# Optimization experiments

Hardware: AMD Instinct MI355X
Metric: run time of the kernel (lower is better)

The kernel has to match this reference:

```python
import jax, jax.numpy as jnp
import numpy as np

EPS = 1e-3


def interpolate_dim(x, n_out):
    # linear interpolation along axis 1, align_corners=True (matches F.interpolate linear)
    n_in = x.shape[1]
    pos = jnp.linspace(0.0, n_in - 1.0, n_out)
    idx0 = jnp.floor(pos).astype(jnp.int32)
    idx1 = jnp.minimum(idx0 + 1, n_in - 1)
    w = (pos - idx0.astype(x.dtype))[None, :, None]
    return x[:, idx0] * (1.0 - w) + x[:, idx1] * w


def logits_to_a_coeff(a_logits, eps):
    # stability-triangle parameterization: |a1| < 2, |a1| - 1 < a2 < 1
    stab = 1.0 - eps
    a1 = 2.0 * jnp.tanh(a_logits[..., 0]) * stab
    a1_abs = jnp.abs(a1)
    a2 = 0.5 * ((2.0 - a1_abs) * jnp.tanh(a_logits[..., 1]) * stab + a1_abs)
    return jnp.stack([a1, a2], axis=-1)  # (B, T, 2)


def sample_wise_lpc(x, a_coeff):
    # time-varying all-pole: y[t] = x[t] - a1[t]*y[t-1] - a2[t]*y[t-2]
    bs = x.shape[0]
    xs = (x.T, a_coeff[..., 0].T, a_coeff[..., 1].T)  # (T, B) each

    def step(carry, inp):
        y1, y2 = carry
        xt, a1, a2 = inp
        y = xt - a1 * y1 - a2 * y2
        return (y, y1), y

    zero = jnp.zeros((bs,), x.dtype)
    _, ys = jax.lax.scan(step, (zero, zero), xs)
    return ys.T  # (B, T)


def time_varying_fir(y, b_coeff):
    # y_out[t] = b0[t]*y[t] + b1[t]*y[t-1] + b2[t]*y[t-2], zero initial conditions
    y_pad = jnp.pad(y, ((0, 0), (2, 0)))
    return (b_coeff[..., 0] * y
            + b_coeff[..., 1] * y_pad[:, 1:-1]
            + b_coeff[..., 2] * y_pad[:, :-2])


def setup_inputs() -> dict:
    key = jax.random.key(0)
    k1, k2 = jax.random.split(key)
    x = jax.random.normal(k1, (32, 262144), dtype=jnp.float32)
    coeff_logits = jax.random.normal(k2, (32, 256, 5), dtype=jnp.float32)
    return {"x": x, "coeff_logits": coeff_logits}


def reference(x, coeff_logits):
    n_samples = x.shape[1]
    # interp_coeff=False: interpolate logits to sample rate first
    logits = interpolate_dim(coeff_logits, n_samples)  # (B, n_samples, 5)
    a_coeff = logits_to_a_coeff(logits[..., :2], EPS)  # (B, n_samples, 2)
    b_coeff = logits[..., 2:]                          # (B, n_samples, 3)
    y_a = sample_wise_lpc(x, a_coeff)
    y_ab = time_varying_fir(y_a, b_coeff)
    return y_ab
```

## Files before the change

kernel.cpp:

```cpp
#include <hip/hip_runtime.h>
#include <math.h>

#define BATCH 32
#define NSAMP 262144
#define NKNOT 256
#define EPSV  0.001f
#define CH    16
#define CPB   256
#define SPB   (CH * CPB)
#define NCROW (NSAMP / CH)
#define BPR   (NCROW / CPB)
#define NB    (BATCH * BPR)
#define NWAVE (CPB / 64)
#define TSTRIDE (CPB + 2)

__device__ __forceinline__ float fast_tanh(float x) {
    float e = __expf(2.0f * x);
    float r = __builtin_amdgcn_rcpf(e + 1.0f);
    return fmaf(-2.0f, r, 1.0f);
}

__global__ __launch_bounds__(256, 4) void k_agg(
    const float* __restrict__ x,
    const float* __restrict__ cl,
    float* __restrict__ G)
{
    __shared__ float tile[CH][TSTRIDE];
    __shared__ float wag[NWAVE][6];
    const int tid = threadIdx.x;
    const int b = blockIdx.x;
    const int lane = tid & 63, wid = tid >> 6;

    const float4* x4 = (const float4*)x + (size_t)b * (SPB / 4);
    #pragma unroll
    for (int i = 0; i < SPB / 4 / CPB; ++i) {
        int ii = tid + i * CPB;
        float4 v = x4[ii];
        int idx = ii << 2;
        int cc = idx >> 4, qq = idx & 15;
        tile[qq + 0][cc] = v.x;
        tile[qq + 1][cc] = v.y;
        tile[qq + 2][cc] = v.z;
        tile[qq + 3][cc] = v.w;
    }

    int chunk = b * CPB + tid;
    int r = chunk >> 14;
    int c = chunk & (NCROW - 1);
    const float scale = 255.0f / 262143.0f;
    float pos0 = (float)(c * CH) * scale;
    float fiA = floorf(pos0);
    int idxA = (int)fiA;
    float w0v = pos0 - fiA;
    const float* kb = cl + (size_t)r * NKNOT * 5;
    int i1 = min(idxA + 1, NKNOT - 1);
    int i2 = min(idxA + 2, NKNOT - 1);
    float k00 = kb[idxA*5+0], k01 = kb[i1*5+0], k02 = kb[i2*5+0];
    float k10 = kb[idxA*5+1], k11 = kb[i1*5+1], k12 = kb[i2*5+1];

    __syncthreads();

    const float stab = 1.0f - EPSV, stab2 = 2.0f * stab;
    float p1 = 0.f, p2 = 0.f, A1 = 1.f, A2 = 0.f, B1 = 0.f, B2 = 1.f;
    #pragma unroll
    for (int j = 0; j < CH; ++j) {
        float xs = tile[j][tid];
        float w = fmaf((float)j, scale, w0v);
        bool sel = w >= 1.0f;
        float wu = sel ? w - 1.0f : w;
        float l0a = sel ? k01 : k00, l0b = sel ? k02 : k01;
        float l1a = sel ? k11 : k10, l1b = sel ? k12 : k11;
        float l0 = fmaf(wu, l0b - l0a, l0a);
        float l1 = fmaf(wu, l1b - l1a, l1a);
        float a1 = stab2 * fast_tanh(l0);
        float a1a = fabsf(a1);
        float a2 = 0.5f * fmaf((2.0f - a1a) * stab, fast_tanh(l1), a1a);
        float p  = fmaf(-a2, p2, xs);  p = fmaf(-a1, p1, p);
        float hA = fmaf(-a1, A1, -a2 * A2);
        float hB = fmaf(-a1, B1, -a2 * B2);
        p2 = p1; p1 = p;
        A2 = A1; A1 = hA;
        B2 = B1; B1 = hB;
    }
    float L00 = A1, L01 = B1, L10 = A2, L11 = B2, Lv0 = p1, Lv1 = p2;

    #pragma unroll
    for (int d = 1; d < 64; d <<= 1) {
        float o00 = __shfl_up(L00, d), o01 = __shfl_up(L01, d);
        float o10 = __shfl_up(L10, d), o11 = __shfl_up(L11, d);
        float ov0 = __shfl_up(Lv0, d), ov1 = __shfl_up(Lv1, d);
        if (lane >= d) {
            float n00 = L00 * o00 + L01 * o10;
            float n01 = L00 * o01 + L01 * o11;
            float n10 = L10 * o00 + L11 * o10;
            float n11 = L10 * o01 + L11 * o11;
            float nv0 = fmaf(L00, ov0, fmaf(L01, ov1, Lv0));
            float nv1 = fmaf(L10, ov0, fmaf(L11, ov1, Lv1));
            L00 = n00; L01 = n01; L10 = n10; L11 = n11; Lv0 = nv0; Lv1 = nv1;
        }
    }
    if (lane == 63) {
        wag[wid][0] = L00; wag[wid][1] = L01; wag[wid][2] = L10;
        wag[wid][3] = L11; wag[wid][4] = Lv0; wag[wid][5] = Lv1;
    }
    __syncthreads();

    if (tid == CPB - 1) {
        float P00 = 1.f, P01 = 0.f, P10 = 0.f, P11 = 1.f, Pv0 = 0.f, Pv1 = 0.f;
        for (int w2 = 0; w2 < NWAVE - 1; ++w2) {
            float a00 = wag[w2][0], a01 = wag[w2][1], a10 = wag[w2][2];
            float a11 = wag[w2][3], av0 = wag[w2][4], av1 = wag[w2][5];
            float n00 = a00 * P00 + a01 * P10;
            float n01 = a00 * P01 + a01 * P11;
            float n10 = a10 * P00 + a11 * P10;
            float n11 = a10 * P01 + a11 * P11;
            float nv0 = fmaf(a00, Pv0, fmaf(a01, Pv1, av0));
            float nv1 = fmaf(a10, Pv0, fmaf(a11, Pv1, av1));
            P00 = n00; P01 = n01; P10 = n10; P11 = n11; Pv0 = nv0; Pv1 = nv1;
        }
        G[b*6+0] = L00 * P00 + L01 * P10;
        G[b*6+1] = L00 * P01 + L01 * P11;
        G[b*6+2] = L10 * P00 + L11 * P10;
        G[b*6+3] = L10 * P01 + L11 * P11;
        G[b*6+4] = fmaf(L00, Pv0, fmaf(L01, Pv1, Lv0));
        G[b*6+5] = fmaf(L10, Pv0, fmaf(L11, Pv1, Lv1));
    }
}

__global__ __launch_bounds__(64) void k_rowscan(
    const float* __restrict__ G,
    float* __restrict__ S)
{
    int r = blockIdx.x;
    int lane = threadIdx.x;
    int rowFirst = r * BPR;
    int k = rowFirst + lane;
    float A00 = G[k*6+0], A01 = G[k*6+1], A10 = G[k*6+2];
    float A11 = G[k*6+3], Av0 = G[k*6+4], Av1 = G[k*6+5];
    #pragma unroll
    for (int d = 1; d < BPR; d <<= 1) {
        float o00 = __shfl_up(A00, d), o01 = __shfl_up(A01, d);
        float o10 = __shfl_up(A10, d), o11 = __shfl_up(A11, d);
        float ov0 = __shfl_up(Av0, d), ov1 = __shfl_up(Av1, d);
        if (lane >= d) {
            float n00 = A00 * o00 + A01 * o10;
            float n01 = A00 * o01 + A01 * o11;
            float n10 = A10 * o00 + A11 * o10;
            float n11 = A10 * o01 + A11 * o11;
            float nv0 = fmaf(A00, ov0, fmaf(A01, ov1, Av0));
            float nv1 = fmaf(A10, ov0, fmaf(A11, ov1, Av1));
            A00 = n00; A01 = n01; A10 = n10; A11 = n11; Av0 = nv0; Av1 = nv1;
        }
    }
    float e0 = __shfl_up(Av0, 1);
    float e1 = __shfl_up(Av1, 1);
    if (lane == 0) { e0 = 0.f; e1 = 0.f; }
    S[k*2 + 0] = e0;
    S[k*2 + 1] = e1;
}

__global__ __launch_bounds__(256, 4) void k_apply(
    const float* __restrict__ x,
    const float* __restrict__ cl,
    const float* __restrict__ S,
    float* __restrict__ out)
{
    __shared__ float tile[CH][TSTRIDE];
    __shared__ float wag[NWAVE][6];
    const int tid = threadIdx.x;
    const int b = blockIdx.x;
    const int lane = tid & 63, wid = tid >> 6;

    const float4* x4 = (const float4*)x + (size_t)b * (SPB / 4);
    #pragma unroll
    for (int i = 0; i < SPB / 4 / CPB; ++i) {
        int ii = tid + i * CPB;
        float4 v = x4[ii];
        int idx = ii << 2;
        int cc = idx >> 4, qq = idx & 15;
        tile[qq + 0][cc] = v.x;
        tile[qq + 1][cc] = v.y;
        tile[qq + 2][cc] = v.z;
        tile[qq + 3][cc] = v.w;
    }

    int chunk = b * CPB + tid;
    int r = chunk >> 14;
    int c = chunk & (NCROW - 1);
    const float scale = 255.0f / 262143.0f;
    float pos0 = (float)(c * CH) * scale;
    float fiA = floorf(pos0);
    int idxA = (int)fiA;
    float w0v = pos0 - fiA;
    const float* kb = cl + (size_t)r * NKNOT * 5;
    int i1 = min(idxA + 1, NKNOT - 1);
    int i2 = min(idxA + 2, NKNOT - 1);
    float k00 = kb[idxA*5+0], k01 = kb[i1*5+0], k02 = kb[i2*5+0];
    float k10 = kb[idxA*5+1], k11 = kb[i1*5+1], k12 = kb[i2*5+1];
    float k20 = kb[idxA*5+2], k21 = kb[i1*5+2], k22 = kb[i2*5+2];
    float k30 = kb[idxA*5+3], k31 = kb[i1*5+3], k32 = kb[i2*5+3];
    float k40 = kb[idxA*5+4], k41 = kb[i1*5+4], k42 = kb[i2*5+4];

    __syncthreads();

    const float stab = 1.0f - EPSV, stab2 = 2.0f * stab;
    float p1 = 0.f, p2 = 0.f, A1 = 1.f, A2 = 0.f, B1 = 0.f, B2 = 1.f;
    #pragma unroll
    for (int j = 0; j < CH; ++j) {
        float xs = tile[j][tid];
        float w = fmaf((float)j, scale, w0v);
        bool sel = w >= 1.0f;
        float wu = sel ? w - 1.0f : w;
        float l0a = sel ? k01 : k00, l0b = sel ? k02 : k01;
        float l1a = sel ? k11 : k10, l1b = sel ? k12 : k11;
        float l0 = fmaf(wu, l0b - l0a, l0a);
        float l1 = fmaf(wu, l1b - l1a, l1a);
        float a1 = stab2 * fast_tanh(l0);
        float a1a = fabsf(a1);
        float a2 = 0.5f * fmaf((2.0f - a1a) * stab, fast_tanh(l1), a1a);
        float p  = fmaf(-a2, p2, xs);  p = fmaf(-a1, p1, p);
        float hA = fmaf(-a1, A1, -a2 * A2);
        float hB = fmaf(-a1, B1, -a2 * B2);
        p2 = p1; p1 = p;
        A2 = A1; A1 = hA;
        B2 = B1; B1 = hB;
    }
    float L00 = A1, L01 = B1, L10 = A2, L11 = B2, Lv0 = p1, Lv1 = p2;

    #pragma unroll
    for (int d = 1; d < 64; d <<= 1) {
        float o00 = __shfl_up(L00, d), o01 = __shfl_up(L01, d);
        float o10 = __shfl_up(L10, d), o11 = __shfl_up(L11, d);
        float ov0 = __shfl_up(Lv0, d), ov1 = __shfl_up(Lv1, d);
        if (lane >= d) {
            float n00 = L00 * o00 + L01 * o10;
            float n01 = L00 * o01 + L01 * o11;
            float n10 = L10 * o00 + L11 * o10;
            float n11 = L10 * o01 + L11 * o11;
            float nv0 = fmaf(L00, ov0, fmaf(L01, ov1, Lv0));
            float nv1 = fmaf(L10, ov0, fmaf(L11, ov1, Lv1));
            L00 = n00; L01 = n01; L10 = n10; L11 = n11; Lv0 = nv0; Lv1 = nv1;
        }
    }
    if (lane == 63) {
        wag[wid][0] = L00; wag[wid][1] = L01; wag[wid][2] = L10;
        wag[wid][3] = L11; wag[wid][4] = Lv0; wag[wid][5] = Lv1;
    }
    __syncthreads();
    float P00 = 1.f, P01 = 0.f, P10 = 0.f, P11 = 1.f, Pv0 = 0.f, Pv1 = 0.f;
    for (int w2 = 0; w2 < wid; ++w2) {
        float a00 = wag[w2][0], a01 = wag[w2][1], a10 = wag[w2][2];
        float a11 = wag[w2][3], av0 = wag[w2][4], av1 = wag[w2][5];
        float n00 = a00 * P00 + a01 * P10;
        float n01 = a00 * P01 + a01 * P11;
        float n10 = a10 * P00 + a11 * P10;
        float n11 = a10 * P01 + a11 * P11;
        float nv0 = fmaf(a00, Pv0, fmaf(a01, Pv1, av0));
        float nv1 = fmaf(a10, Pv0, fmaf(a11, Pv1, av1));
        P00 = n00; P01 = n01; P10 = n10; P11 = n11; Pv0 = nv0; Pv1 = nv1;
    }
    float E00 = __shfl_up(L00, 1), E01 = __shfl_up(L01, 1);
    float E10 = __shfl_up(L10, 1), E11 = __shfl_up(L11, 1);
    float Ev0 = __shfl_up(Lv0, 1), Ev1 = __shfl_up(Lv1, 1);
    if (lane == 0) { E00 = 1.f; E01 = 0.f; E10 = 0.f; E11 = 1.f; Ev0 = 0.f; Ev1 = 0.f; }
    float C00 = E00 * P00 + E01 * P10;
    float C01 = E00 * P01 + E01 * P11;
    float C10 = E10 * P00 + E11 * P10;
    float C11 = E10 * P01 + E11 * P11;
    float Cv0 = fmaf(E00, Pv0, fmaf(E01, Pv1, Ev0));
    float Cv1 = fmaf(E10, Pv0, fmaf(E11, Pv1, Ev1));

    float s0 = S[b*2+0], s1 = S[b*2+1];
    float y1 = fmaf(C00, s0, fmaf(C01, s1, Cv0));
    float y2 = fmaf(C10, s0, fmaf(C11, s1, Cv1));

    #pragma unroll
    for (int j = 0; j < CH; ++j) {
        float xs = tile[j][tid];
        float w = fmaf((float)j, scale, w0v);
        bool sel = w >= 1.0f;
        float wu = sel ? w - 1.0f : w;
        float l0a = sel ? k01 : k00, l0b = sel ? k02 : k01;
        float l1a = sel ? k11 : k10, l1b = sel ? k12 : k11;
        float b0a = sel ? k21 : k20, b0b = sel ? k22 : k21;
        float b1a = sel ? k31 : k30, b1b = sel ? k32 : k31;
        float b2a = sel ? k41 : k40, b2b = sel ? k42 : k41;
        float l0 = fmaf(wu, l0b - l0a, l0a);
        float l1 = fmaf(wu, l1b - l1a, l1a);
        float b0 = fmaf(wu, b0b - b0a, b0a);
        float b1 = fmaf(wu, b1b - b1a, b1a);
        float b2 = fmaf(wu, b2b - b2a, b2a);
        float a1 = stab2 * fast_tanh(l0);
        float a1a = fabsf(a1);
        float a2 = 0.5f * fmaf((2.0f - a1a) * stab, fast_tanh(l1), a1a);
        float y = fmaf(-a2, y2, xs);  y = fmaf(-a1, y1, y);
        tile[j][tid] = fmaf(b0, y, fmaf(b1, y1, b2 * y2));
        y2 = y1; y1 = y;
    }
    __syncthreads();

    float4* out4 = (float4*)out + (size_t)b * (SPB / 4);
    #pragma unroll
    for (int i = 0; i < SPB / 4 / CPB; ++i) {
        int ii = tid + i * CPB;
        int idx = ii << 2;
        int cc = idx >> 4, qq = idx & 15;
        float4 v;
        v.x = tile[qq + 0][cc];
        v.y = tile[qq + 1][cc];
        v.z = tile[qq + 2][cc];
        v.w = tile[qq + 3][cc];
        out4[ii] = v;
    }
}

extern "C" void kernel_launch(void* const* d_in, const int* in_sizes, int n_in,
                              void* d_out, int out_size, void* d_ws, size_t ws_size,
                              hipStream_t stream) {
    const float* x  = (const float*)d_in[0];
    const float* cl = (const float*)d_in[1];
    float* out = (float*)d_out;
    float* G = (float*)d_ws;
    float* S = G + (size_t)NB * 6;

    hipLaunchKernelGGL(k_agg,     dim3(NB),    dim3(CPB), 0, stream, x, cl, G);
    hipLaunchKernelGGL(k_rowscan, dim3(BATCH), dim3(64),  0, stream, G, S);
    hipLaunchKernelGGL(k_apply,   dim3(NB),    dim3(CPB), 0, stream, x, cl, S, out);
}
```

Baseline: 42.68 us.

## Fuse row scan into apply, use exp recurrence for tanh, row-major float4 LDS tile

The separate row-scan kernel is removed, and every apply block's first wave redoes the 64-block prefix scan over the aggregates, which are now stored in SoA layout. This saves one launch and its serialization at the cost of redundant work. Per-sample tanh now multiplies the exponential by a constant ratio inside each knot segment instead of calling expf per sample, replacing the exp with a multiply. The LDS tile moves to a padded row-per-thread layout so threads use float4 reads and writes. The recurrent exp product may add small float drift.

```diff
diff --git a/kernel.cpp b/kernel.cpp
--- a/kernel.cpp
+++ b/kernel.cpp
@@ -12,20 +12,14 @@
 #define BPR   (NCROW / CPB)
 #define NB    (BATCH * BPR)
 #define NWAVE (CPB / 64)
-#define TSTRIDE (CPB + 2)
-
-__device__ __forceinline__ float fast_tanh(float x) {
-    float e = __expf(2.0f * x);
-    float r = __builtin_amdgcn_rcpf(e + 1.0f);
-    return fmaf(-2.0f, r, 1.0f);
-}
+#define ROWW  20
 
 __global__ __launch_bounds__(256, 4) void k_agg(
     const float* __restrict__ x,
     const float* __restrict__ cl,
     float* __restrict__ G)
 {
-    __shared__ float tile[CH][TSTRIDE];
+    __shared__ float tile[CPB * ROWW];
     __shared__ float wag[NWAVE][6];
     const int tid = threadIdx.x;
     const int b = blockIdx.x;
@@ -33,15 +27,10 @@
 
     const float4* x4 = (const float4*)x + (size_t)b * (SPB / 4);
     #pragma unroll
-    for (int i = 0; i < SPB / 4 / CPB; ++i) {
+    for (int i = 0; i < 4; ++i) {
         int ii = tid + i * CPB;
         float4 v = x4[ii];
-        int idx = ii << 2;
-        int cc = idx >> 4, qq = idx & 15;
-        tile[qq + 0][cc] = v.x;
-        tile[qq + 1][cc] = v.y;
-        tile[qq + 2][cc] = v.z;
-        tile[qq + 3][cc] = v.w;
+        *(float4*)&tile[(ii >> 2) * ROWW + ((ii & 3) << 2)] = v;
     }
 
     int chunk = b * CPB + tid;
@@ -58,29 +47,54 @@
     float k00 = kb[idxA*5+0], k01 = kb[i1*5+0], k02 = kb[i2*5+0];
     float k10 = kb[idxA*5+1], k11 = kb[i1*5+1], k12 = kb[i2*5+1];
 
+    int jb = 0;
+    #pragma unroll
+    for (int j = 0; j < CH; ++j) jb += (fmaf((float)j, scale, w0v) < 1.0f) ? 1 : 0;
+
+    float dA0 = k01 - k00, dB0 = k02 - k01;
+    float dA1 = k11 - k10, dB1 = k12 - k11;
+    float wb  = fmaf((float)jb, scale, w0v) - 1.0f;
+    float eA0 = __expf(2.0f * fmaf(w0v, dA0, k00));
+    float EA0 = __expf(2.0f * scale * dA0);
+    float eB0 = __expf(2.0f * fmaf(wb,  dB0, k01));
+    float EB0 = __expf(2.0f * scale * dB0);
+    float eA1 = __expf(2.0f * fmaf(w0v, dA1, k10));
+    float EA1 = __expf(2.0f * scale * dA1);
+    float eB1 = __expf(2.0f * fmaf(wb,  dB1, k11));
+    float EB1 = __expf(2.0f * scale * dB1);
+
     __syncthreads();
 
     const float stab = 1.0f - EPSV, stab2 = 2.0f * stab;
     float p1 = 0.f, p2 = 0.f, A1 = 1.f, A2 = 0.f, B1 = 0.f, B2 = 1.f;
-    #pragma unroll
-    for (int j = 0; j < CH; ++j) {
-        float xs = tile[j][tid];
-        float w = fmaf((float)j, scale, w0v);
-        bool sel = w >= 1.0f;
-        float wu = sel ? w - 1.0f : w;
-        float l0a = sel ? k01 : k00, l0b = sel ? k02 : k01;
-        float l1a = sel ? k11 : k10, l1b = sel ? k12 : k11;
-        float l0 = fmaf(wu, l0b - l0a, l0a);
-        float l1 = fmaf(wu, l1b - l1a, l1a);
-        float a1 = stab2 * fast_tanh(l0);
-        float a1a = fabsf(a1);
-        float a2 = 0.5f * fmaf((2.0f - a1a) * stab, fast_tanh(l1), a1a);
-        float p  = fmaf(-a2, p2, xs);  p = fmaf(-a1, p1, p);
-        float hA = fmaf(-a1, A1, -a2 * A2);
-        float hB = fmaf(-a1, B1, -a2 * B2);
-        p2 = p1; p1 = p;
-        A2 = A1; A1 = hA;
-        B2 = B1; B1 = hB;
+    float e0 = eA0, e1 = eA1;
+    #pragma unroll
+    for (int jj = 0; jj < CH / 4; ++jj) {
+        float4 xq = *(const float4*)&tile[tid * ROWW + (jj << 2)];
+        #pragma unroll
+        for (int q = 0; q < 4; ++q) {
+            const int j = jj * 4 + q;
+            if (j > 0) {
+                float m0 = (j <= jb) ? EA0 : EB0;
+                float m1 = (j <= jb) ? EA1 : EB1;
+                e0 = (j == jb) ? eB0 : e0 * m0;
+                e1 = (j == jb) ? eB1 : e1 * m1;
+            }
+            float r0 = __builtin_amdgcn_rcpf(e0 + 1.0f);
+            float r1 = __builtin_amdgcn_rcpf(e1 + 1.0f);
+            float th0 = fmaf(-2.0f, r0, 1.0f);
+            float th1 = fmaf(-2.0f, r1, 1.0f);
+            float a1 = stab2 * th0;
+            float a1a = fabsf(a1);
+            float a2 = 0.5f * fmaf((2.0f - a1a) * stab, th1, a1a);
+            float xs = (&xq.x)[q];
+            float p  = fmaf(-a2, p2, xs);  p = fmaf(-a1, p1, p);
+            float hA = fmaf(-a1, A1, -a2 * A2);
+            float hB = fmaf(-a1, B1, -a2 * B2);
+            p2 = p1; p1 = p;
+            A2 = A1; A1 = hA;
+            B2 = B1; B1 = hB;
+        }
     }
     float L00 = A1, L01 = B1, L10 = A2, L11 = B2, Lv0 = p1, Lv1 = p2;
 
@@ -118,70 +132,64 @@
             float nv1 = fmaf(a10, Pv0, fmaf(a11, Pv1, av1));
             P00 = n00; P01 = n01; P10 = n10; P11 = n11; Pv0 = nv0; Pv1 = nv1;
         }
-        G[b*6+0] = L00 * P00 + L01 * P10;
-        G[b*6+1] = L00 * P01 + L01 * P11;
-        G[b*6+2] = L10 * P00 + L11 * P10;
-        G[b*6+3] = L10 * P01 + L11 * P11;
-        G[b*6+4] = fmaf(L00, Pv0, fmaf(L01, Pv1, Lv0));
-        G[b*6+5] = fmaf(L10, Pv0, fmaf(L11, Pv1, Lv1));
-    }
-}
-
-__global__ __launch_bounds__(64) void k_rowscan(
-    const float* __restrict__ G,
-    float* __restrict__ S)
-{
-    int r = blockIdx.x;
-    int lane = threadIdx.x;
-    int rowFirst = r * BPR;
-    int k = rowFirst + lane;
-    float A00 = G[k*6+0], A01 = G[k*6+1], A10 = G[k*6+2];
-    float A11 = G[k*6+3], Av0 = G[k*6+4], Av1 = G[k*6+5];
-    #pragma unroll
-    for (int d = 1; d < BPR; d <<= 1) {
-        float o00 = __shfl_up(A00, d), o01 = __shfl_up(A01, d);
-        float o10 = __shfl_up(A10, d), o11 = __shfl_up(A11, d);
-        float ov0 = __shfl_up(Av0, d), ov1 = __shfl_up(Av1, d);
-        if (lane >= d) {
-            float n00 = A00 * o00 + A01 * o10;
-            float n01 = A00 * o01 + A01 * o11;
-            float n10 = A10 * o00 + A11 * o10;
-            float n11 = A10 * o01 + A11 * o11;
-            float nv0 = fmaf(A00, ov0, fmaf(A01, ov1, Av0));
-            float nv1 = fmaf(A10, ov0, fmaf(A11, ov1, Av1));
-            A00 = n00; A01 = n01; A10 = n10; A11 = n11; Av0 = nv0; Av1 = nv1;
-        }
-    }
-    float e0 = __shfl_up(Av0, 1);
-    float e1 = __shfl_up(Av1, 1);
-    if (lane == 0) { e0 = 0.f; e1 = 0.f; }
-    S[k*2 + 0] = e0;
-    S[k*2 + 1] = e1;
+        G[0*NB + b] = L00 * P00 + L01 * P10;
+        G[1*NB + b] = L00 * P01 + L01 * P11;
+        G[2*NB + b] = L10 * P00 + L11 * P10;
+        G[3*NB + b] = L10 * P01 + L11 * P11;
+        G[4*NB + b] = fmaf(L00, Pv0, fmaf(L01, Pv1, Lv0));
+        G[5*NB + b] = fmaf(L10, Pv0, fmaf(L11, Pv1, Lv1));
+    }
 }
 
 __global__ __launch_bounds__(256, 4) void k_apply(
     const float* __restrict__ x,
     const float* __restrict__ cl,
-    const float* __restrict__ S,
+    const float* __restrict__ G,
     float* __restrict__ out)
 {
-    __shared__ float tile[CH][TSTRIDE];
+    __shared__ float tile[CPB * ROWW];
     __shared__ float wag[NWAVE][6];
+    __shared__ float sInit[2];
     const int tid = threadIdx.x;
     const int b = blockIdx.x;
     const int lane = tid & 63, wid = tid >> 6;
 
     const float4* x4 = (const float4*)x + (size_t)b * (SPB / 4);
     #pragma unroll
-    for (int i = 0; i < SPB / 4 / CPB; ++i) {
+    for (int i = 0; i < 4; ++i) {
         int ii = tid + i * CPB;
         float4 v = x4[ii];
-        int idx = ii << 2;
-        int cc = idx >> 4, qq = idx & 15;
-        tile[qq + 0][cc] = v.x;
-        tile[qq + 1][cc] = v.y;
-        tile[qq + 2][cc] = v.z;
-        tile[qq + 3][cc] = v.w;
+        *(float4*)&tile[(ii >> 2) * ROWW + ((ii & 3) << 2)] = v;
+    }
+
+    if (wid == 0) {
+        int rowFirst = b & ~(BPR - 1);
+        int k = rowFirst + lane;
+        float A00 = G[0*NB + k], A01 = G[1*NB + k], A10 = G[2*NB + k];
+        float A11 = G[3*NB + k], Av0 = G[4*NB + k], Av1 = G[5*NB + k];
+        #pragma unroll
+        for (int d = 1; d < 64; d <<= 1) {
+            float o00 = __shfl_up(A00, d), o01 = __shfl_up(A01, d);
+            float o10 = __shfl_up(A10, d), o11 = __shfl_up(A11, d);
+            float ov0 = __shfl_up(Av0, d), ov1 = __shfl_up(Av1, d);
+            if (lane >= d) {
+                float n00 = A00 * o00 + A01 * o10;
+                float n01 = A00 * o01 + A01 * o11;
+                float n10 = A10 * o00 + A11 * o10;
+                float n11 = A10 * o01 + A11 * o11;
+                float nv0 = fmaf(A00, ov0, fmaf(A01, ov1, Av0));
+                float nv1 = fmaf(A10, ov0, fmaf(A11, ov1, Av1));
+                A00 = n00; A01 = n01; A10 = n10; A11 = n11; Av0 = nv0; Av1 = nv1;
+            }
+        }
+        int myIdx = b & (BPR - 1);
+        int src = (myIdx > 0) ? myIdx - 1 : 0;
+        float s0 = __shfl(Av0, src);
+        float s1 = __shfl(Av1, src);
+        if (lane == 0) {
+            sInit[0] = myIdx ? s0 : 0.f;
+            sInit[1] = myIdx ? s1 : 0.f;
+        }
     }
 
     int chunk = b * CPB + tid;
@@ -201,29 +209,54 @@
     float k30 = kb[idxA*5+3], k31 = kb[i1*5+3], k32 = kb[i2*5+3];
     float k40 = kb[idxA*5+4], k41 = kb[i1*5+4], k42 = kb[i2*5+4];
 
+    int jb = 0;
+    #pragma unroll
+    for (int j = 0; j < CH; ++j) jb += (fmaf((float)j, scale, w0v) < 1.0f) ? 1 : 0;
+
+    float dA0 = k01 - k00, dB0 = k02 - k01;
+    float dA1 = k11 - k10, dB1 = k12 - k11;
+    float wb  = fmaf((float)jb, scale, w0v) - 1.0f;
+    float eA0 = __expf(2.0f * fmaf(w0v, dA0, k00));
+    float EA0 = __expf(2.0f * scale * dA0);
+    float eB0 = __expf(2.0f * fmaf(wb,  dB0, k01));
+    float EB0 = __expf(2.0f * scale * dB0);
+    float eA1 = __expf(2.0f * fmaf(w0v, dA1, k10));
+    float EA1 = __expf(2.0f * scale * dA1);
+    float eB1 = __expf(2.0f * fmaf(wb,  dB1, k11));
+    float EB1 = __expf(2.0f * scale * dB1);
+
     __syncthreads();
 
     const float stab = 1.0f - EPSV, stab2 = 2.0f * stab;
     float p1 = 0.f, p2 = 0.f, A1 = 1.f, A2 = 0.f, B1 = 0.f, B2 = 1.f;
-    #pragma unroll
-    for (int j = 0; j < CH; ++j) {
-        float xs = tile[j][tid];
-        float w = fmaf((float)j, scale, w0v);
-        bool sel = w >= 1.0f;
-        float wu = sel ? w - 1.0f : w;
-        float l0a = sel ? k01 : k00, l0b = sel ? k02 : k01;
-        float l1a = sel ? k11 : k10, l1b = sel ? k12 : k11;
-        float l0 = fmaf(wu, l0b - l0a, l0a);
-        float l1 = fmaf(wu, l1b - l1a, l1a);
-        float a1 = stab2 * fast_tanh(l0);
-        float a1a = fabsf(a1);
-        float a2 = 0.5f * fmaf((2.0f - a1a) * stab, fast_tanh(l1), a1a);
-        float p  = fmaf(-a2, p2, xs);  p = fmaf(-a1, p1, p);
-        float hA = fmaf(-a1, A1, -a2 * A2);
-        float hB = fmaf(-a1, B1, -a2 * B2);
-        p2 = p1; p1 = p;
-        A2 = A1; A1 = hA;
-        B2 = B1; B1 = hB;
+    float e0 = eA0, e1 = eA1;
+    #pragma unroll
+    for (int jj = 0; jj < CH / 4; ++jj) {
+        float4 xq = *(const float4*)&tile[tid * ROWW + (jj << 2)];
+        #pragma unroll
+        for (int q = 0; q < 4; ++q) {
+            const int j = jj * 4 + q;
+            if (j > 0) {
+                float m0 = (j <= jb) ? EA0 : EB0;
+                float m1 = (j <= jb) ? EA1 : EB1;
+                e0 = (j == jb) ? eB0 : e0 * m0;
+                e1 = (j == jb) ? eB1 : e1 * m1;
+            }
+            float r0 = __builtin_amdgcn_rcpf(e0 + 1.0f);
+            float r1 = __builtin_amdgcn_rcpf(e1 + 1.0f);
+            float th0 = fmaf(-2.0f, r0, 1.0f);
+            float th1 = fmaf(-2.0f, r1, 1.0f);
+            float a1 = stab2 * th0;
+            float a1a = fabsf(a1);
+            float a2 = 0.5f * fmaf((2.0f - a1a) * stab, th1, a1a);
+            float xs = (&xq.x)[q];
+            float p  = fmaf(-a2, p2, xs);  p = fmaf(-a1, p1, p);
+            float hA = fmaf(-a1, A1, -a2 * A2);
+            float hB = fmaf(-a1, B1, -a2 * B2);
+            p2 = p1; p1 = p;
+            A2 = A1; A1 = hA;
+            B2 = B1; B1 = hB;
+        }
     }
     float L00 = A1, L01 = B1, L10 = A2, L11 = B2, Lv0 = p1, Lv1 = p2;
 
@@ -270,47 +303,52 @@
     float Cv0 = fmaf(E00, Pv0, fmaf(E01, Pv1, Ev0));
     float Cv1 = fmaf(E10, Pv0, fmaf(E11, Pv1, Ev1));
 
-    float s0 = S[b*2+0], s1 = S[b*2+1];
+    float s0 = sInit[0], s1 = sInit[1];
     float y1 = fmaf(C00, s0, fmaf(C01, s1, Cv0));
     float y2 = fmaf(C10, s0, fmaf(C11, s1, Cv1));
 
-    #pragma unroll
-    for (int j = 0; j < CH; ++j) {
-        float xs = tile[j][tid];
-        float w = fmaf((float)j, scale, w0v);
-        bool sel = w >= 1.0f;
-        float wu = sel ? w - 1.0f : w;
-        float l0a = sel ? k01 : k00, l0b = sel ? k02 : k01;
-        float l1a = sel ? k11 : k10, l1b = sel ? k12 : k11;
-        float b0a = sel ? k21 : k20, b0b = sel ? k22 : k21;
-        float b1a = sel ? k31 : k30, b1b = sel ? k32 : k31;
-        float b2a = sel ? k41 : k40, b2b = sel ? k42 : k41;
-        float l0 = fmaf(wu, l0b - l0a, l0a);
-        float l1 = fmaf(wu, l1b - l1a, l1a);
-        float b0 = fmaf(wu, b0b - b0a, b0a);
-        float b1 = fmaf(wu, b1b - b1a, b1a);
-        float b2 = fmaf(wu, b2b - b2a, b2a);
-        float a1 = stab2 * fast_tanh(l0);
-        float a1a = fabsf(a1);
-        float a2 = 0.5f * fmaf((2.0f - a1a) * stab, fast_tanh(l1), a1a);
-        float y = fmaf(-a2, y2, xs);  y = fmaf(-a1, y1, y);
-        tile[j][tid] = fmaf(b0, y, fmaf(b1, y1, b2 * y2));
-        y2 = y1; y1 = y;
+    e0 = eA0; e1 = eA1;
+    #pragma unroll
+    for (int jj = 0; jj < CH / 4; ++jj) {
+        float* tp = &tile[tid * ROWW + (jj << 2)];
+        float4 xq = *(const float4*)tp;
+        float4 ov;
+        #pragma unroll
+        for (int q = 0; q < 4; ++q) {
+            const int j = jj * 4 + q;
+            if (j > 0) {
+                float m0 = (j <= jb) ? EA0 : EB0;
+                float m1 = (j <= jb) ? EA1 : EB1;
+                e0 = (j == jb) ? eB0 : e0 * m0;
+                e1 = (j == jb) ? eB1 : e1 * m1;
+            }
+            float r0 = __builtin_amdgcn_rcpf(e0 + 1.0f);
+            float r1 = __builtin_amdgcn_rcpf(e1 + 1.0f);
+            float th0 = fmaf(-2.0f, r0, 1.0f);
+            float th1 = fmaf(-2.0f, r1, 1.0f);
+            float a1 = stab2 * th0;
+            float a1a = fabsf(a1);
+            float a2 = 0.5f * fmaf((2.0f - a1a) * stab, th1, a1a);
+            float w = fmaf((float)j, scale, w0v);
+            bool isB = (j >= jb);
+            float wu = isB ? w - 1.0f : w;
+            float b0 = fmaf(wu, isB ? (k22-k21) : (k21-k20), isB ? k21 : k20);
+            float b1c = fmaf(wu, isB ? (k32-k31) : (k31-k30), isB ? k31 : k30);
+            float b2c = fmaf(wu, isB ? (k42-k41) : (k41-k40), isB ? k41 : k40);
+            float xs = (&xq.x)[q];
+            float y = fmaf(-a2, y2, xs);  y = fmaf(-a1, y1, y);
+            (&ov.x)[q] = fmaf(b0, y, fmaf(b1c, y1, b2c * y2));
+            y2 = y1; y1 = y;
+        }
+        *(float4*)tp = ov;
     }
     __syncthreads();
 
     float4* out4 = (float4*)out + (size_t)b * (SPB / 4);
     #pragma unroll
-    for (int i = 0; i < SPB / 4 / CPB; ++i) {
+    for (int i = 0; i < 4; ++i) {
         int ii = tid + i * CPB;
-        int idx = ii << 2;
-        int cc = idx >> 4, qq = idx & 15;
-        float4 v;
-        v.x = tile[qq + 0][cc];
-        v.y = tile[qq + 1][cc];
-        v.z = tile[qq + 2][cc];
-        v.w = tile[qq + 3][cc];
-        out4[ii] = v;
+        out4[ii] = *(const float4*)&tile[(ii >> 2) * ROWW + ((ii & 3) << 2)];
     }
 }
 
@@ -321,9 +359,7 @@
     const float* cl = (const float*)d_in[1];
     float* out = (float*)d_out;
     float* G = (float*)d_ws;
-    float* S = G + (size_t)NB * 6;
-
-    hipLaunchKernelGGL(k_agg,     dim3(NB),    dim3(CPB), 0, stream, x, cl, G);
-    hipLaunchKernelGGL(k_rowscan, dim3(BATCH), dim3(64),  0, stream, G, S);
-    hipLaunchKernelGGL(k_apply,   dim3(NB),    dim3(CPB), 0, stream, x, cl, S, out);
+
+    hipLaunchKernelGGL(k_agg,   dim3(NB), dim3(CPB), 0, stream, x, cl, G);
+    hipLaunchKernelGGL(k_apply, dim3(NB), dim3(CPB), 0, stream, x, cl, G, out);
 }
```

After: 42.73 us. About the same (+0.1%).

## Fold row scan into apply kernel and load x directly into registers

Applied to the files above, without the earlier changes.

Removes the separate k_rowscan launch. Each k_apply block's first wave now redoes the 64-entry per-row prefix scan of block aggregates, read from a structure-of-arrays G layout, and shares the carry-in through LDS. Both kernels drop the LDS transpose tile: each thread loads its 16 contiguous samples with four float4 loads and writes its outputs the same way, which also removes the tile barriers. Interpolation slopes are precomputed outside the loop. The costs are redundant scan work in every block and strided per-lane global accesses that are less coalesced than the tiled version.

```diff
diff --git a/kernel.cpp b/kernel.cpp
--- a/kernel.cpp
+++ b/kernel.cpp
@@ -7,12 +7,10 @@
 #define EPSV  0.001f
 #define CH    16
 #define CPB   256
-#define SPB   (CH * CPB)
 #define NCROW (NSAMP / CH)
 #define BPR   (NCROW / CPB)
 #define NB    (BATCH * BPR)
 #define NWAVE (CPB / 64)
-#define TSTRIDE (CPB + 2)
 
 __device__ __forceinline__ float fast_tanh(float x) {
     float e = __expf(2.0f * x);
@@ -25,26 +23,19 @@
     const float* __restrict__ cl,
     float* __restrict__ G)
 {
-    __shared__ float tile[CH][TSTRIDE];
     __shared__ float wag[NWAVE][6];
     const int tid = threadIdx.x;
     const int b = blockIdx.x;
     const int lane = tid & 63, wid = tid >> 6;
 
-    const float4* x4 = (const float4*)x + (size_t)b * (SPB / 4);
-    #pragma unroll
-    for (int i = 0; i < SPB / 4 / CPB; ++i) {
-        int ii = tid + i * CPB;
-        float4 v = x4[ii];
-        int idx = ii << 2;
-        int cc = idx >> 4, qq = idx & 15;
-        tile[qq + 0][cc] = v.x;
-        tile[qq + 1][cc] = v.y;
-        tile[qq + 2][cc] = v.z;
-        tile[qq + 3][cc] = v.w;
-    }
-
     int chunk = b * CPB + tid;
+    const float4* xp = (const float4*)(x + (size_t)chunk * CH);
+    float xr[CH];
+    *(float4*)&xr[0]  = xp[0];
+    *(float4*)&xr[4]  = xp[1];
+    *(float4*)&xr[8]  = xp[2];
+    *(float4*)&xr[12] = xp[3];
+
     int r = chunk >> 14;
     int c = chunk & (NCROW - 1);
     const float scale = 255.0f / 262143.0f;
@@ -57,25 +48,22 @@
     int i2 = min(idxA + 2, NKNOT - 1);
     float k00 = kb[idxA*5+0], k01 = kb[i1*5+0], k02 = kb[i2*5+0];
     float k10 = kb[idxA*5+1], k11 = kb[i1*5+1], k12 = kb[i2*5+1];
-
-    __syncthreads();
+    float d0A = k01-k00, d0B = k02-k01;
+    float d1A = k11-k10, d1B = k12-k11;
 
     const float stab = 1.0f - EPSV, stab2 = 2.0f * stab;
     float p1 = 0.f, p2 = 0.f, A1 = 1.f, A2 = 0.f, B1 = 0.f, B2 = 1.f;
     #pragma unroll
     for (int j = 0; j < CH; ++j) {
-        float xs = tile[j][tid];
         float w = fmaf((float)j, scale, w0v);
         bool sel = w >= 1.0f;
         float wu = sel ? w - 1.0f : w;
-        float l0a = sel ? k01 : k00, l0b = sel ? k02 : k01;
-        float l1a = sel ? k11 : k10, l1b = sel ? k12 : k11;
-        float l0 = fmaf(wu, l0b - l0a, l0a);
-        float l1 = fmaf(wu, l1b - l1a, l1a);
+        float l0 = fmaf(wu, sel ? d0B : d0A, sel ? k01 : k00);
+        float l1 = fmaf(wu, sel ? d1B : d1A, sel ? k11 : k10);
         float a1 = stab2 * fast_tanh(l0);
         float a1a = fabsf(a1);
         float a2 = 0.5f * fmaf((2.0f - a1a) * stab, fast_tanh(l1), a1a);
-        float p  = fmaf(-a2, p2, xs);  p = fmaf(-a1, p1, p);
+        float p  = fmaf(-a2, p2, xr[j]);  p = fmaf(-a1, p1, p);
         float hA = fmaf(-a1, A1, -a2 * A2);
         float hB = fmaf(-a1, B1, -a2 * B2);
         p2 = p1; p1 = p;
@@ -118,73 +106,65 @@
             float nv1 = fmaf(a10, Pv0, fmaf(a11, Pv1, av1));
             P00 = n00; P01 = n01; P10 = n10; P11 = n11; Pv0 = nv0; Pv1 = nv1;
         }
-        G[b*6+0] = L00 * P00 + L01 * P10;
-        G[b*6+1] = L00 * P01 + L01 * P11;
-        G[b*6+2] = L10 * P00 + L11 * P10;
-        G[b*6+3] = L10 * P01 + L11 * P11;
-        G[b*6+4] = fmaf(L00, Pv0, fmaf(L01, Pv1, Lv0));
-        G[b*6+5] = fmaf(L10, Pv0, fmaf(L11, Pv1, Lv1));
-    }
-}
-
-__global__ __launch_bounds__(64) void k_rowscan(
-    const float* __restrict__ G,
-    float* __restrict__ S)
-{
-    int r = blockIdx.x;
-    int lane = threadIdx.x;
-    int rowFirst = r * BPR;
-    int k = rowFirst + lane;
-    float A00 = G[k*6+0], A01 = G[k*6+1], A10 = G[k*6+2];
-    float A11 = G[k*6+3], Av0 = G[k*6+4], Av1 = G[k*6+5];
-    #pragma unroll
-    for (int d = 1; d < BPR; d <<= 1) {
-        float o00 = __shfl_up(A00, d), o01 = __shfl_up(A01, d);
-        float o10 = __shfl_up(A10, d), o11 = __shfl_up(A11, d);
-        float ov0 = __shfl_up(Av0, d), ov1 = __shfl_up(Av1, d);
-        if (lane >= d) {
-            float n00 = A00 * o00 + A01 * o10;
-            float n01 = A00 * o01 + A01 * o11;
-            float n10 = A10 * o00 + A11 * o10;
-            float n11 = A10 * o01 + A11 * o11;
-            float nv0 = fmaf(A00, ov0, fmaf(A01, ov1, Av0));
-            float nv1 = fmaf(A10, ov0, fmaf(A11, ov1, Av1));
-            A00 = n00; A01 = n01; A10 = n10; A11 = n11; Av0 = nv0; Av1 = nv1;
-        }
-    }
-    float e0 = __shfl_up(Av0, 1);
-    float e1 = __shfl_up(Av1, 1);
-    if (lane == 0) { e0 = 0.f; e1 = 0.f; }
-    S[k*2 + 0] = e0;
-    S[k*2 + 1] = e1;
+        G[0*NB + b] = L00 * P00 + L01 * P10;
+        G[1*NB + b] = L00 * P01 + L01 * P11;
+        G[2*NB + b] = L10 * P00 + L11 * P10;
+        G[3*NB + b] = L10 * P01 + L11 * P11;
+        G[4*NB + b] = fmaf(L00, Pv0, fmaf(L01, Pv1, Lv0));
+        G[5*NB + b] = fmaf(L10, Pv0, fmaf(L11, Pv1, Lv1));
+    }
 }
 
 __global__ __launch_bounds__(256, 4) void k_apply(
     const float* __restrict__ x,
     const float* __restrict__ cl,
-    const float* __restrict__ S,
+    const float* __restrict__ G,
     float* __restrict__ out)
 {
-    __shared__ float tile[CH][TSTRIDE];
     __shared__ float wag[NWAVE][6];
+    __shared__ float sInit[2];
     const int tid = threadIdx.x;
     const int b = blockIdx.x;
     const int lane = tid & 63, wid = tid >> 6;
 
-    const float4* x4 = (const float4*)x + (size_t)b * (SPB / 4);
-    #pragma unroll
-    for (int i = 0; i < SPB / 4 / CPB; ++i) {
-        int ii = tid + i * CPB;
-        float4 v = x4[ii];
-        int idx = ii << 2;
-        int cc = idx >> 4, qq = idx & 15;
-        tile[qq + 0][cc] = v.x;
-        tile[qq + 1][cc] = v.y;
-        tile[qq + 2][cc] = v.z;
-        tile[qq + 3][cc] = v.w;
+    if (wid == 0) {
+        int rowFirst = b & ~(BPR - 1);
+        int k = rowFirst + lane;
+        float A00 = G[0*NB + k], A01 = G[1*NB + k], A10 = G[2*NB + k];
+        float A11 = G[3*NB + k], Av0 = G[4*NB + k], Av1 = G[5*NB + k];
+        #pragma unroll
+        for (int d = 1; d < 64; d <<= 1) {
+            float o00 = __shfl_up(A00, d), o01 = __shfl_up(A01, d);
+            float o10 = __shfl_up(A10, d), o11 = __shfl_up(A11, d);
+            float ov0 = __shfl_up(Av0, d), ov1 = __shfl_up(Av1, d);
+            if (lane >= d) {
+                float n00 = A00 * o00 + A01 * o10;
+                float n01 = A00 * o01 + A01 * o11;
+                float n10 = A10 * o00 + A11 * o10;
+                float n11 = A10 * o01 + A11 * o11;
+                float nv0 = fmaf(A00, ov0, fmaf(A01, ov1, Av0));
+                float nv1 = fmaf(A10, ov0, fmaf(A11, ov1, Av1));
+                A00 = n00; A01 = n01; A10 = n10; A11 = n11; Av0 = nv0; Av1 = nv1;
+            }
+        }
+        int myIdx = b & (BPR - 1);
+        int src = (myIdx > 0) ? myIdx - 1 : 0;
+        float s0 = __shfl(Av0, src);
+        float s1 = __shfl(Av1, src);
+        if (lane == 0) {
+            sInit[0] = myIdx ? s0 : 0.f;
+            sInit[1] = myIdx ? s1 : 0.f;
+        }
     }
 
     int chunk = b * CPB + tid;
+    const float4* xp = (const float4*)(x + (size_t)chunk * CH);
+    float xr[CH];
+    *(float4*)&xr[0]  = xp[0];
+    *(float4*)&xr[4]  = xp[1];
+    *(float4*)&xr[8]  = xp[2];
+    *(float4*)&xr[12] = xp[3];
+
     int r = chunk >> 14;
     int c = chunk & (NCROW - 1);
     const float scale = 255.0f / 262143.0f;
@@ -200,25 +180,25 @@
     float k20 = kb[idxA*5+2], k21 = kb[i1*5+2], k22 = kb[i2*5+2];
     float k30 = kb[idxA*5+3], k31 = kb[i1*5+3], k32 = kb[i2*5+3];
     float k40 = kb[idxA*5+4], k41 = kb[i1*5+4], k42 = kb[i2*5+4];
-
-    __syncthreads();
+    float d0A = k01-k00, d0B = k02-k01;
+    float d1A = k11-k10, d1B = k12-k11;
+    float d2A = k21-k20, d2B = k22-k21;
+    float d3A = k31-k30, d3B = k32-k31;
+    float d4A = k41-k40, d4B = k42-k41;
 
     const float stab = 1.0f - EPSV, stab2 = 2.0f * stab;
     float p1 = 0.f, p2 = 0.f, A1 = 1.f, A2 = 0.f, B1 = 0.f, B2 = 1.f;
     #pragma unroll
     for (int j = 0; j < CH; ++j) {
-        float xs = tile[j][tid];
         float w = fmaf((float)j, scale, w0v);
         bool sel = w >= 1.0f;
         float wu = sel ? w - 1.0f : w;
-        float l0a = sel ? k01 : k00, l0b = sel ? k02 : k01;
-        float l1a = sel ? k11 : k10, l1b = sel ? k12 : k11;
-        float l0 = fmaf(wu, l0b - l0a, l0a);
-        float l1 = fmaf(wu, l1b - l1a, l1a);
+        float l0 = fmaf(wu, sel ? d0B : d0A, sel ? k01 : k00);
+        float l1 = fmaf(wu, sel ? d1B : d1A, sel ? k11 : k10);
         float a1 = stab2 * fast_tanh(l0);
         float a1a = fabsf(a1);
         float a2 = 0.5f * fmaf((2.0f - a1a) * stab, fast_tanh(l1), a1a);
-        float p  = fmaf(-a2, p2, xs);  p = fmaf(-a1, p1, p);
+        float p  = fmaf(-a2, p2, xr[j]);  p = fmaf(-a1, p1, p);
         float hA = fmaf(-a1, A1, -a2 * A2);
         float hB = fmaf(-a1, B1, -a2 * B2);
         p2 = p1; p1 = p;
@@ -270,48 +250,33 @@
     float Cv0 = fmaf(E00, Pv0, fmaf(E01, Pv1, Ev0));
     float Cv1 = fmaf(E10, Pv0, fmaf(E11, Pv1, Ev1));
 
-    float s0 = S[b*2+0], s1 = S[b*2+1];
+    float s0 = sInit[0], s1 = sInit[1];
     float y1 = fmaf(C00, s0, fmaf(C01, s1, Cv0));
     float y2 = fmaf(C10, s0, fmaf(C11, s1, Cv1));
 
     #pragma unroll
     for (int j = 0; j < CH; ++j) {
-        float xs = tile[j][tid];
         float w = fmaf((float)j, scale, w0v);
         bool sel = w >= 1.0f;
         float wu = sel ? w - 1.0f : w;
-        float l0a = sel ? k01 : k00, l0b = sel ? k02 : k01;
-        float l1a = sel ? k11 : k10, l1b = sel ? k12 : k11;
-        float b0a = sel ? k21 : k20, b0b = sel ? k22 : k21;
-        float b1a = sel ? k31 : k30, b1b = sel ? k32 : k31;
-        float b2a = sel ? k41 : k40, b2b = sel ? k42 : k41;
-        float l0 = fmaf(wu, l0b - l0a, l0a);
-        float l1 = fmaf(wu, l1b - l1a, l1a);
-        float b0 = fmaf(wu, b0b - b0a, b0a);
-        float b1 = fmaf(wu, b1b - b1a, b1a);
-        float b2 = fmaf(wu, b2b - b2a, b2a);
+        float l0 = fmaf(wu, sel ? d0B : d0A, sel ? k01 : k00);
+        float l1 = fmaf(wu, sel ? d1B : d1A, sel ? k11 : k10);
+        float b0 = fmaf(wu, sel ? d2B : d2A, sel ? k21 : k20);
+        float b1c= fmaf(wu, sel ? d3B : d3A, sel ? k31 : k30);
+        float b2c= fmaf(wu, sel ? d4B : d4A, sel ? k41 : k40);
         float a1 = stab2 * fast_tanh(l0);
         float a1a = fabsf(a1);
         float a2 = 0.5f * fmaf((2.0f - a1a) * stab, fast_tanh(l1), a1a);
-        float y = fmaf(-a2, y2, xs);  y = fmaf(-a1, y1, y);
-        tile[j][tid] = fmaf(b0, y, fmaf(b1, y1, b2 * y2));
+        float y = fmaf(-a2, y2, xr[j]);  y = fmaf(-a1, y1, y);
+        xr[j] = fmaf(b0, y, fmaf(b1c, y1, b2c * y2));
         y2 = y1; y1 = y;
     }
-    __syncthreads();
-
-    float4* out4 = (float4*)out + (size_t)b * (SPB / 4);
-    #pragma unroll
-    for (int i = 0; i < SPB / 4 / CPB; ++i) {
-        int ii = tid + i * CPB;
-        int idx = ii << 2;
-        int cc = idx >> 4, qq = idx & 15;
-        float4 v;
-        v.x = tile[qq + 0][cc];
-        v.y = tile[qq + 1][cc];
-        v.z = tile[qq + 2][cc];
-        v.w = tile[qq + 3][cc];
-        out4[ii] = v;
-    }
+
+    float4* op = (float4*)(out + (size_t)chunk * CH);
+    op[0] = *(const float4*)&xr[0];
+    op[1] = *(const float4*)&xr[4];
+    op[2] = *(const float4*)&xr[8];
+    op[3] = *(const float4*)&xr[12];
 }
 
 extern "C" void kernel_launch(void* const* d_in, const int* in_sizes, int n_in,
@@ -321,9 +286,7 @@
     const float* cl = (const float*)d_in[1];
     float* out = (float*)d_out;
     float* G = (float*)d_ws;
-    float* S = G + (size_t)NB * 6;
-
-    hipLaunchKernelGGL(k_agg,     dim3(NB),    dim3(CPB), 0, stream, x, cl, G);
-    hipLaunchKernelGGL(k_rowscan, dim3(BATCH), dim3(64),  0, stream, G, S);
-    hipLaunchKernelGGL(k_apply,   dim3(NB),    dim3(CPB), 0, stream, x, cl, S, out);
-}
+
+    hipLaunchKernelGGL(k_agg,   dim3(NB), dim3(CPB), 0, stream, x, cl, G);
+    hipLaunchKernelGGL(k_apply, dim3(NB), dim3(CPB), 0, stream, x, cl, G, out);
+}
```

New measurement: 40.61 us. 4.9% less time.
